# Kernel optimization log

Measured on AMD Instinct MI355X. Metric: run time of the kernel, lower is better.

## Reference

```python
import jax, jax.numpy as jnp
import numpy as np

NUM_HEADS = 8
EPS = 1e-5


def _dwconv_cpe(x, w, b, H, W):
    # x: [B,N,C]; depthwise 3x3 conv positional encoding with residual
    B, N, C = x.shape
    f = x.transpose(0, 2, 1).reshape(B, C, H, W)
    f = jax.lax.conv_general_dilated(
        f, w, window_strides=(1, 1), padding='SAME',
        feature_group_count=C, dimension_numbers=('NCHW', 'OIHW', 'NCHW'))
    f = f + b[None, :, None, None]
    return x + f.reshape(B, C, N).transpose(0, 2, 1)


def _layernorm(x, g, b):
    mu = jnp.mean(x, axis=-1, keepdims=True)
    var = jnp.mean(jnp.square(x - mu), axis=-1, keepdims=True)
    return (x - mu) * jax.lax.rsqrt(var + EPS) * g + b


def _channel_attn(x, source, q_w, kv_w, proj_w, proj_b):
    B, N, C = x.shape
    h = NUM_HEADS
    d = C // h
    scale = d ** -0.5
    q = (x @ q_w).reshape(B, N, h, d).transpose(0, 2, 1, 3)          # [B,h,N,d]
    kv = (source @ kv_w).reshape(B, N, 2, h, d).transpose(2, 0, 3, 1, 4)
    k = kv[0] * scale                                                # [B,h,N,d]
    v = kv[1]                                                        # [B,h,N,d]
    # channel cross-covariance: [B,h,d,d], softmax over last channel dim
    attn = jax.nn.softmax(jnp.einsum('bhnd,bhne->bhde', k, v), axis=-1)
    out = jnp.einsum('bhde,bhne->bhnd', attn, q)                     # [B,h,N,d]
    out = out.transpose(0, 2, 1, 3).reshape(B, N, C)
    return out @ proj_w + proj_b


def _forward(x, source, H, W, cpe0_w, cpe0_b, cpe1_w, cpe1_b,
             norm1_g, norm1_b, q_w, kv_w, proj_w, proj_b,
             norm2_g, norm2_b, fc1_w, fc1_b, fc2_w, fc2_b):
    x = _dwconv_cpe(x, cpe0_w, cpe0_b, H, W)
    source = _dwconv_cpe(source, cpe0_w, cpe0_b, H, W)  # cpe[0] shared, per source
    x = _layernorm(x, norm1_g, norm1_b)
    source = _layernorm(source, norm1_g, norm1_b)
    cur = _channel_attn(x, source, q_w, kv_w, proj_w, proj_b)
    x = x + cur  # residual on the normalized x (as in the original code)
    x = _dwconv_cpe(x, cpe1_w, cpe1_b, H, W)
    h = _layernorm(x, norm2_g, norm2_b)
    h = jax.nn.gelu(h @ fc1_w + fc1_b, approximate=False) @ fc2_w + fc2_b
    return x + h


def setup_inputs() -> dict:
    key = jax.random.key(0)
    ks = jax.random.split(key, 16)
    B, H, W, C = 8, 64, 64, 384
    N = H * W
    Ch = int(C * 4.0)
    s = 0.02
    return {
        'x': jax.random.normal(ks[0], (B, N, C), jnp.float32),
        'source': jax.random.normal(ks[1], (B, N, C), jnp.float32),
        'H': H, 'W': W,
        'cpe0_w': jax.random.normal(ks[2], (C, 1, 3, 3), jnp.float32) * s,
        'cpe0_b': jnp.zeros((C,), jnp.float32),
        'cpe1_w': jax.random.normal(ks[3], (C, 1, 3, 3), jnp.float32) * s,
        'cpe1_b': jnp.zeros((C,), jnp.float32),
        'norm1_g': jnp.ones((C,), jnp.float32),
        'norm1_b': jnp.zeros((C,), jnp.float32),
        'q_w': jax.random.normal(ks[4], (C, C), jnp.float32) * s,
        'kv_w': jax.random.normal(ks[5], (C, 2 * C), jnp.float32) * s,
        'proj_w': jax.random.normal(ks[6], (C, C), jnp.float32) * s,
        'proj_b': jnp.zeros((C,), jnp.float32),
        'norm2_g': jnp.ones((C,), jnp.float32),
        'norm2_b': jnp.zeros((C,), jnp.float32),
        'fc1_w': jax.random.normal(ks[7], (C, Ch), jnp.float32) * s,
        'fc1_b': jnp.zeros((Ch,), jnp.float32),
        'fc2_w': jax.random.normal(ks[8], (Ch, C), jnp.float32) * s,
        'fc2_b': jnp.zeros((C,), jnp.float32),
    }


def reference(x, source, H, W, cpe0_w, cpe0_b, cpe1_w, cpe1_b,
              norm1_g, norm1_b, q_w, kv_w, proj_w, proj_b,
              norm2_g, norm2_b, fc1_w, fc1_b, fc2_w, fc2_b):
    return _forward(x, source, H, W, cpe0_w, cpe0_b, cpe1_w, cpe1_b,
                    norm1_g, norm1_b, q_w, kv_w, proj_w, proj_b,
                    norm2_g, norm2_b, fc1_w, fc1_b, fc2_w, fc2_b)
```

## Files before the change

kernel.cpp:

```cpp
#include <hip/hip_runtime.h>
#include <hip/hip_bf16.h>
#include <math.h>

typedef __hip_bfloat16 bf16;
typedef unsigned short u16t;
typedef __bf16 bfx8 __attribute__((ext_vector_type(8)));
typedef float fx4 __attribute__((ext_vector_type(4)));
typedef unsigned short usx8 __attribute__((ext_vector_type(8)));

constexpr int Bq = 8, Hh = 64, Ww = 64, Nn = 4096, Cc = 384, NH = 8, CH = 1536;
constexpr int Mrows = Bq * Nn;
constexpr int NS = 4;
constexpr int NSP = 6;
constexpr float EPSC = 1e-5f;
constexpr float SCALE = 0.14433756729740643f;

__device__ __forceinline__ float toF(bf16 v) { return __bfloat162float(v); }

__device__ __forceinline__ float ldFlag(const void* p, size_t i, int f) {
    if (f) return __bfloat162float(((const bf16*)p)[i]);
    return ((const float*)p)[i];
}

__device__ __forceinline__ float u2f(u16t u) {
    unsigned int x = ((unsigned int)u) << 16;
    float fv;
    __builtin_memcpy(&fv, &x, 4);
    return fv;
}
__device__ __forceinline__ u16t f2u(float v) {
    bf16 h = __float2bfloat16(v);
    u16t u;
    __builtin_memcpy(&u, &h, 2);
    return u;
}
__device__ __forceinline__ fx4 mfma16(usx8 a, usx8 b, fx4 c) {
    return __builtin_amdgcn_mfma_f32_16x16x32_bf16(
        __builtin_bit_cast(bfx8, a), __builtin_bit_cast(bfx8, b), c, 0, 0, 0);
}

__device__ __forceinline__ void gload16(const void* g, void* l) {
    __builtin_amdgcn_global_load_lds(
        reinterpret_cast<const __attribute__((address_space(1))) unsigned int*>(
            reinterpret_cast<uintptr_t>(g)),
        reinterpret_cast<__attribute__((address_space(3))) unsigned int*>(
            reinterpret_cast<uintptr_t>(l)),
        16, 0, 0);
}

__global__ __launch_bounds__(256) void probe_k(const void* __restrict__ p, int* __restrict__ flag) {
    int t = threadIdx.x;
    int bad = 0;
    for (int i = t; i < 4096; i += 256) {
        unsigned short u = ((const unsigned short*)p)[i];
        unsigned e = (u >> 7) & 0xFF;
        if (e >= 134) bad++;
    }
    __shared__ int sh[256];
    sh[t] = bad;
    __syncthreads();
    for (int s = 128; s > 0; s >>= 1) {
        if (t < s) sh[t] += sh[t + s];
        __syncthreads();
    }
    if (t == 0) flag[0] = (sh[0] < 64) ? 1 : 0;
}

template <int INM, int MODE>
__global__ __launch_bounds__(384) void dwconv_ln(const void* __restrict__ xin,
                                                 const void* __restrict__ w,
                                                 const void* __restrict__ bias,
                                                 bf16* __restrict__ out,
                                                 const void* __restrict__ g,
                                                 const void* __restrict__ bb,
                                                 float* __restrict__ mu,
                                                 float* __restrict__ rs,
                                                 const int* __restrict__ flagp) {
    int f = *flagp;
    int c = threadIdx.x;
    int w0 = blockIdx.x * 8;
    int hh = blockIdx.y;
    int b = blockIdx.z;
    size_t base = (size_t)b * Nn * Cc;
    float wreg[9];
#pragma unroll
    for (int j = 0; j < 9; j++) wreg[j] = ldFlag(w, c * 9 + j, f);
    float bc = ldFlag(bias, c, f);
    float v[3][10];
#pragma unroll
    for (int ky = 0; ky < 3; ky++) {
        int yy = hh + ky - 1;
        bool rv = (yy >= 0 && yy < Hh);
#pragma unroll
        for (int j = 0; j < 10; j++) {
            int xx = w0 - 1 + j;
            bool cv = (xx >= 0 && xx < Ww);
            float val = 0.f;
            if (rv && cv) {
                size_t idx = base + (size_t)(yy * Ww + xx) * Cc + c;
                val = (INM == 1) ? toF(((const bf16*)xin)[idx]) : ldFlag(xin, idx, f);
            }
            v[ky][j] = val;
        }
    }
    float r[8], s[8], s2[8];
#pragma unroll
    for (int p = 0; p < 8; p++) {
        float a = bc;
#pragma unroll
        for (int ky = 0; ky < 3; ky++)
#pragma unroll
            for (int kx = 0; kx < 3; kx++) a += v[ky][p + kx] * wreg[ky * 3 + kx];
        r[p] = v[1][p + 1] + a;
        s[p] = r[p];
        s2[p] = r[p] * r[p];
    }
#pragma unroll
    for (int off = 32; off > 0; off >>= 1) {
#pragma unroll
        for (int p = 0; p < 8; p++) {
            s[p] += __shfl_down(s[p], off, 64);
            s2[p] += __shfl_down(s2[p], off, 64);
        }
    }
    __shared__ float shS[6][8], shS2[6][8];
    __shared__ float shMu[8], shRs[8];
    int wv = c >> 6, ln = c & 63;
    if (ln == 0) {
#pragma unroll
        for (int p = 0; p < 8; p++) {
            shS[wv][p] = s[p];
            shS2[wv][p] = s2[p];
        }
    }
    __syncthreads();
    if (c < 8) {
        float S = 0, S2 = 0;
#pragma unroll
        for (int q = 0; q < 6; q++) {
            S += shS[q][c];
            S2 += shS2[q][c];
        }
        float m = S * (1.0f / Cc);
        float var = S2 * (1.0f / Cc) - m * m;
        float rr = rsqrtf(var + EPSC);
        if (MODE == 0) {
            shMu[c] = m;
            shRs[c] = rr;
        } else {
            int row = b * Nn + hh * Ww + w0 + c;
            mu[row] = m;
            rs[row] = rr;
        }
    }
    if (MODE == 0) {
        __syncthreads();
        float gc = ldFlag(g, c, f), bbc = ldFlag(bb, c, f);
#pragma unroll
        for (int p = 0; p < 8; p++) {
            size_t oi = base + (size_t)(hh * Ww + w0 + p) * Cc + c;
            out[oi] = __float2bfloat16((r[p] - shMu[p]) * shRs[p] * gc + bbc);
        }
    } else {
#pragma unroll
        for (int p = 0; p < 8; p++) {
            size_t oi = base + (size_t)(hh * Ww + w0 + p) * Cc + c;
            out[oi] = __float2bfloat16(r[p]);
        }
    }
}

__global__ __launch_bounds__(256) void reduceG_k(float* __restrict__ Gp) {
    const size_t Q = (size_t)Cc * Cc / 4;
    size_t j = (size_t)blockIdx.x * 256 + threadIdx.x;
    int b = (int)(j / Q);
    size_t i4 = j % Q;
    fx4* G4 = (fx4*)Gp;
    size_t base = (size_t)b * NS * Q;
    fx4 a = G4[base + i4];
#pragma unroll
    for (int s = 1; s < NS; s++) a += G4[base + (size_t)s * Q + i4];
    G4[base + i4] = a;
}

template <int AM, int OM, int WM, bool GELU, bool LNA, int RES, int AR>
__global__ __launch_bounds__(256) void gemm_k(const void* __restrict__ A, size_t aBatch,
                                              const void* __restrict__ W, size_t wBatch,
                                              int ldw, int colOff,
                                              const void* __restrict__ bias,
                                              const bf16* __restrict__ resid, size_t rBatch,
                                              const float* __restrict__ mu,
                                              const float* __restrict__ rs, size_t sBatch,
                                              const void* __restrict__ cg,
                                              const void* __restrict__ cb,
                                              void* __restrict__ out, size_t oBatch,
                                              size_t outRow0,
                                              int M, int K, int Nc,
                                              const int* __restrict__ flagp) {
    int f = *flagp;
    int z = blockIdx.z;
    const size_t MK = (size_t)M * K;
    __shared__ float As[16][68];
    __shared__ float Bs[16][68];
    int t = threadIdx.x;
    int tx = t & 15, ty = t >> 4;
    int row0 = blockIdx.x * 64, n0 = blockIdx.y * 64;
    float acc[4][4] = {};
    for (int k0 = 0; k0 < K; k0 += 16) {
#pragma unroll
        for (int i = 0; i < 4; i++) {
            int lin = i * 256 + t;
            int kk = lin & 15, m = lin >> 4;
            size_t ai = (size_t)z * aBatch + (size_t)(row0 + m) * K + k0 + kk;
            float v;
            if (AR > 1) {
                v = 0;
#pragma unroll
                for (int s = 0; s < AR; s++) v += ((const float*)A)[ai + (size_t)s * MK];
            } else {
                v = (AM == 0) ? ((const float*)A)[ai] : toF(((const bf16*)A)[ai]);
            }
            if (LNA) {
                float muv = mu[z * sBatch + row0 + m], rsv = rs[z * sBatch + row0 + m];
                v = (v - muv) * rsv * ldFlag(cg, k0 + kk, f) + ldFlag(cb, k0 + kk, f);
            }
            As[kk][m] = v;
        }
#pragma unroll
        for (int i = 0; i < 4; i++) {
            int lin = i * 256 + t;
            int nn2 = lin & 63, kk = lin >> 6;
            size_t wi = (size_t)z * wBatch + (size_t)(k0 + kk) * ldw + colOff + n0 + nn2;
            Bs[kk][nn2] = (WM == 1) ? toF(((const bf16*)W)[wi]) : ldFlag(W, wi, f);
        }
        __syncthreads();
#pragma unroll
        for (int kk = 0; kk < 16; kk++) {
            float a[4], bv[4];
#pragma unroll
            for (int i = 0; i < 4; i++) a[i] = As[kk][ty * 4 + i];
#pragma unroll
            for (int j = 0; j < 4; j++) bv[j] = Bs[kk][tx * 4 + j];
#pragma unroll
            for (int i = 0; i < 4; i++)
#pragma unroll
                for (int j = 0; j < 4; j++) acc[i][j] += a[i] * bv[j];
        }
        __syncthreads();
    }
#pragma unroll
    for (int i = 0; i < 4; i++) {
        int m = row0 + ty * 4 + i;
#pragma unroll
        for (int j = 0; j < 4; j++) {
            int nn2 = n0 + tx * 4 + j;
            float v = acc[i][j];
            if (bias) v += ldFlag(bias, nn2, f);
            if (GELU) v = 0.5f * v * (1.0f + erff(v * 0.70710678118654752f));
            if (RES == 1) v += toF(resid[(size_t)z * rBatch + (size_t)m * Nc + nn2]);
            size_t oi = (size_t)z * oBatch + (outRow0 + m) * (size_t)Nc + nn2;
            if (OM == 2) ((float*)out)[oi] = v;
            else if (OM == 1) ((bf16*)out)[oi] = __float2bfloat16(v);
            else {
                if (f) ((bf16*)out)[oi] = __float2bfloat16(v);
                else ((float*)out)[oi] = v;
            }
        }
    }
}

__global__ __launch_bounds__(256) void transpose_k(const void* __restrict__ W,
                                                   u16t* __restrict__ WT,
                                                   int K, int N,
                                                   const int* __restrict__ flagp) {
    int f = *flagp;
    __shared__ u16t T[64][72];
    int n0 = blockIdx.x * 64, k0 = blockIdx.y * 64;
    int t = threadIdx.x;
#pragma unroll
    for (int i = 0; i < 16; i++) {
        int lin = i * 256 + t;
        int kk = lin >> 6, nn = lin & 63;
        T[nn][kk] = f2u(ldFlag(W, (size_t)(k0 + kk) * N + n0 + nn, f));
    }
    __syncthreads();
#pragma unroll
    for (int i = 0; i < 16; i++) {
        int lin = i * 256 + t;
        int nn = lin >> 6, kk = lin & 63;
        WT[(size_t)(n0 + nn) * K + k0 + kk] = T[nn][kk];
    }
}

__global__ __launch_bounds__(256) void transpose_scale_k(const void* __restrict__ W,
                                                         const void* __restrict__ g,
                                                         u16t* __restrict__ WT,
                                                         int K, int N,
                                                         const int* __restrict__ flagp) {
    int f = *flagp;
    __shared__ u16t T[64][72];
    int n0 = blockIdx.x * 64, k0 = blockIdx.y * 64;
    int t = threadIdx.x;
#pragma unroll
    for (int i = 0; i < 16; i++) {
        int lin = i * 256 + t;
        int kk = lin >> 6, nn = lin & 63;
        T[nn][kk] = f2u(ldFlag(g, k0 + kk, f) * ldFlag(W, (size_t)(k0 + kk) * N + n0 + nn, f));
    }
    __syncthreads();
#pragma unroll
    for (int i = 0; i < 16; i++) {
        int lin = i * 256 + t;
        int nn = lin >> 6, kk = lin & 63;
        WT[(size_t)(n0 + nn) * K + k0 + kk] = T[nn][kk];
    }
}

__global__ __launch_bounds__(256) void fc1fold_k(const void* __restrict__ fc1w,
                                                 const void* __restrict__ g,
                                                 const void* __restrict__ bb,
                                                 const void* __restrict__ b1,
                                                 float* __restrict__ negc1,
                                                 float* __restrict__ cb2,
                                                 const int* __restrict__ flagp) {
    int f = *flagp;
    __shared__ float gs[384], bs[384];
    int t = threadIdx.x;
    for (int i = t; i < 384; i += 256) {
        gs[i] = ldFlag(g, i, f);
        bs[i] = ldFlag(bb, i, f);
    }
    __syncthreads();
    int n = blockIdx.x * 256 + t;
    float s1 = 0, s2 = 0;
    for (int k = 0; k < 384; k++) {
        float w = ldFlag(fc1w, (size_t)k * CH + n, f);
        s1 += gs[k] * w;
        s2 += bs[k] * w;
    }
    negc1[n] = -s1;
    cb2[n] = s2 + ldFlag(b1, n, f);
}

template <int OM, bool GELU, int RES, int EPI>
__global__ __launch_bounds__(256) void gemm_mfma(
    const u16t* __restrict__ A, size_t aBatch,
    const u16t* __restrict__ BT, size_t btBatch,
    const void* __restrict__ bias,
    const u16t* __restrict__ resid, size_t rBatch,
    const float* __restrict__ mu, const float* __restrict__ rs,
    const float* __restrict__ negc1, const float* __restrict__ cb2,
    void* __restrict__ out, size_t oBatch, size_t outRow0,
    int K, int N, const int* __restrict__ flagp) {
    int f = *flagp;
    int z = blockIdx.z;
    int t = threadIdx.x;
    int row0 = blockIdx.x * 128, n0 = blockIdx.y * 128;
    __shared__ u16t As[128][64];
    __shared__ u16t Bs[128][64];
    const u16t* Ab = A + (size_t)z * aBatch;
    const u16t* Bb = BT + (size_t)z * btBatch;
    int lane = t & 63, wv = t >> 6;
    int srow = lane >> 3;
    int schk = ((lane & 7) ^ srow) << 3;
    const u16t* asrc[4];
    const u16t* bsrc[4];
    u16t* adst[4];
    u16t* bdst[4];
#pragma unroll
    for (int i = 0; i < 4; i++) {
        int r = 32 * wv + 8 * i;
        asrc[i] = Ab + (size_t)(row0 + r + srow) * K + schk;
        bsrc[i] = Bb + (size_t)(n0 + r + srow) * K + schk;
        adst[i] = &As[r][0];
        bdst[i] = &Bs[r][0];
    }
    fx4 acc[4][4];
    fx4 zz = {0.f, 0.f, 0.f, 0.f};
#pragma unroll
    for (int i = 0; i < 4; i++)
#pragma unroll
        for (int j = 0; j < 4; j++) acc[i][j] = zz;
    int wr = (wv >> 1) * 64, wc = (wv & 1) * 64;
    int lr = lane & 15, lg = lane >> 4;
    int KT = K / 64;
    for (int kt = 0; kt < KT; kt++) {
        if (kt) __syncthreads();
#pragma unroll
        for (int i = 0; i < 4; i++) {
            gload16(asrc[i] + kt * 64, adst[i]);
            gload16(bsrc[i] + kt * 64, bdst[i]);
        }
        __syncthreads();
#pragma unroll
        for (int ks = 0; ks < 2; ks++) {
            usx8 af[4], bfv[4];
#pragma unroll
            for (int r = 0; r < 4; r++) {
                int row = wr + r * 16 + lr;
                af[r] = *(const usx8*)&As[row][((4 * ks + lg) ^ (row & 7)) << 3];
            }
#pragma unroll
            for (int c = 0; c < 4; c++) {
                int row = wc + c * 16 + lr;
                bfv[c] = *(const usx8*)&Bs[row][((4 * ks + lg) ^ (row & 7)) << 3];
            }
#pragma unroll
            for (int r = 0; r < 4; r++)
#pragma unroll
                for (int c = 0; c < 4; c++)
                    acc[r][c] = mfma16(af[r], bfv[c], acc[r][c]);
        }
    }
#pragma unroll
    for (int r = 0; r < 4; r++) {
        int mb = row0 + wr + r * 16 + lg * 4;
        fx4 muq, rsq;
        if (EPI == 1) {
            muq = *(const fx4*)&mu[mb];
            rsq = *(const fx4*)&rs[mb];
        }
#pragma unroll
        for (int c = 0; c < 4; c++) {
            int gc = n0 + wc + c * 16 + lr;
            float bv = bias ? ldFlag(bias, gc, f) : 0.0f;
            float nc1 = (EPI == 1) ? negc1[gc] : 0.f;
            float cbv = (EPI == 1) ? cb2[gc] : 0.f;
#pragma unroll
            for (int q = 0; q < 4; q++) {
                int m = mb + q;
                float v;
                if (EPI == 1) v = rsq[q] * (acc[r][c][q] + muq[q] * nc1) + cbv;
                else v = acc[r][c][q] + bv;
                if (GELU) v = 0.5f * v * (1.0f + erff(v * 0.70710678118654752f));
                if (RES == 1) v += u2f(resid[(size_t)z * rBatch + (size_t)m * N + gc]);
                if (RES == 2) v += u2f(Ab[(size_t)m * K + gc]);
                size_t oi = (size_t)z * oBatch + (outRow0 + m) * (size_t)N + gc;
                if (OM == 1) ((u16t*)out)[oi] = f2u(v);
                else {
                    if (f) ((u16t*)out)[oi] = f2u(v);
                    else ((float*)out)[oi] = v;
                }
            }
        }
    }
}

__global__ __launch_bounds__(256) void gram_mfma(const u16t* __restrict__ sc,
                                                 float* __restrict__ Gp) {
    int bx = blockIdx.x, sp = blockIdx.y, b = blockIdx.z;
    int ci0 = (bx / 3) * 128, cj0 = (bx % 3) * 128;
    __shared__ u16t As[128][72];
    __shared__ u16t Bs[128][72];
    int t = threadIdx.x;
    const int scc = (t * 8) & 127;
    const int snn = t >> 4;
    const int RPS = Nn / NS;
    int rowbase = b * Nn + sp * RPS;
    usx8 ra[4], rb[4];
    auto ldstep = [&](int nn0) {
#pragma unroll
        for (int i = 0; i < 4; i++) {
            int r = rowbase + nn0 + i * 16 + snn;
            ra[i] = *(const usx8*)&sc[(size_t)r * Cc + ci0 + scc];
            rb[i] = *(const usx8*)&sc[(size_t)r * Cc + cj0 + scc];
        }
    };
    auto wrstep = [&]() {
#pragma unroll
        for (int i = 0; i < 4; i++) {
            int n = i * 16 + snn;
            int q = n >> 3, nl = n & 7;
#pragma unroll
            for (int j = 0; j < 8; j++) {
                int c = scc + j;
                int swz = ((c >> 3) ^ (c >> 6)) & 7;
                int po = ((q ^ swz) << 3) + nl;
                As[c][po] = ra[i][j];
                Bs[c][po] = rb[i][j];
            }
        }
    };
    fx4 acc[4][4];
    fx4 zz = {0.f, 0.f, 0.f, 0.f};
#pragma unroll
    for (int i = 0; i < 4; i++)
#pragma unroll
        for (int j = 0; j < 4; j++) acc[i][j] = zz;
    int lane = t & 63, w = t >> 6;
    int wr = (w >> 1) * 64, wc = (w & 1) * 64;
    int lr = lane & 15, lg = lane >> 4;
    ldstep(0);
    wrstep();
    __syncthreads();
    const int KT = RPS / 64;
    for (int kt = 0; kt < KT; kt++) {
        if (kt + 1 < KT) ldstep((kt + 1) * 64);
#pragma unroll
        for (int ks = 0; ks < 2; ks++) {
            usx8 af[4], bfv[4];
#pragma unroll
            for (int r = 0; r < 4; r++) {
                int ch = wr + r * 16 + lr;
                int swz = ((ch >> 3) ^ (ch >> 6)) & 7;
                af[r] = *(const usx8*)&As[ch][((ks * 4 + lg) ^ swz) << 3];
            }
#pragma unroll
            for (int c = 0; c < 4; c++) {
                int ch = wc + c * 16 + lr;
                int swz = ((ch >> 3) ^ (ch >> 6)) & 7;
                bfv[c] = *(const usx8*)&Bs[ch][((ks * 4 + lg) ^ swz) << 3];
            }
#pragma unroll
            for (int r = 0; r < 4; r++)
#pragma unroll
                for (int c = 0; c < 4; c++)
                    acc[r][c] = mfma16(af[r], bfv[c], acc[r][c]);
        }
        __syncthreads();
        if (kt + 1 < KT) {
            wrstep();
            __syncthreads();
        }
    }
    float* dst = Gp + ((size_t)b * NS + sp) * (size_t)Cc * Cc;
#pragma unroll
    for (int r = 0; r < 4; r++)
#pragma unroll
        for (int c = 0; c < 4; c++)
#pragma unroll
            for (int q = 0; q < 4; q++)
                dst[(size_t)(ci0 + wr + r * 16 + lg * 4 + q) * Cc + cj0 + wc + c * 16 + lr] =
                    acc[r][c][q];
}

__global__ __launch_bounds__(256) void attn_part_k(const float* __restrict__ P,
                                                   const void* __restrict__ kv_w,
                                                   float* __restrict__ Sp,
                                                   const int* __restrict__ flagp) {
    int f = *flagp;
    int hd = blockIdx.x;
    int b = blockIdx.y;
    int sp = blockIdx.z;
    int c0 = sp * 64;
    int t = threadIdx.x;
    const float* Pb = P + (size_t)b * Cc * Cc;
    __shared__ float Pc[64][49];
    __shared__ float Wkc[64][49];
    for (int idx = t; idx < 3072; idx += 256) {
        int r = idx / 48, e = idx % 48;
        int c = c0 + r;
        Pc[r][e] = Pb[(size_t)c * Cc + hd * 48 + e];
        Wkc[r][e] = ldFlag(kv_w, (size_t)c * 768 + hd * 48 + e, f);
    }
    __syncthreads();
    int obase = t * 9;
    float acc[9] = {};
#pragma unroll
    for (int r = 0; r < 64; r++) {
#pragma unroll
        for (int j = 0; j < 9; j++) {
            int d = (obase + j) / 48, e = (obase + j) % 48;
            acc[j] += Wkc[r][d] * Pc[r][e];
        }
    }
    float* dst = Sp + (((size_t)b * NH + hd) * NSP + sp) * 2304;
#pragma unroll
    for (int j = 0; j < 9; j++) dst[obase + j] = acc[j];
}

__global__ __launch_bounds__(256) void attn_soft_k(const float* __restrict__ Sp,
                                                   float* __restrict__ attn) {
    int hd = blockIdx.x;
    int b = blockIdx.y;
    int t = threadIdx.x;
    __shared__ float Ss[48][49];
    const float* src = Sp + (((size_t)b * NH + hd) * NSP) * 2304;
    for (int idx = t; idx < 2304; idx += 256) {
        float s = 0;
#pragma unroll
        for (int sp = 0; sp < NSP; sp++) s += src[sp * 2304 + idx];
        Ss[idx / 48][idx % 48] = s * SCALE;
    }
    __syncthreads();
    if (t < 48) {
        float m = -1e30f;
#pragma unroll
        for (int e = 0; e < 48; e++) m = fmaxf(m, Ss[t][e]);
        float ex[48];
        float sum = 0;
#pragma unroll
        for (int e = 0; e < 48; e++) {
            ex[e] = expf(Ss[t][e] - m);
            sum += ex[e];
        }
        float inv = 1.0f / sum;
#pragma unroll
        for (int e = 0; e < 48; e++)
            attn[((size_t)b * NH + hd) * 2304 + t * 48 + e] = ex[e] * inv;
    }
}

__global__ __launch_bounds__(256) void wtilde_k(const void* __restrict__ q_w,
                                                const float* __restrict__ attn,
                                                bf16* __restrict__ Wt_,
                                                const int* __restrict__ flagp) {
    int f = *flagp;
    int c0 = blockIdx.x * 64;
    int hd = blockIdx.y;
    int b = blockIdx.z;
    int t = threadIdx.x;
    __shared__ float at[48][48];
    __shared__ float wq[64][48];
    const float* ab = attn + ((size_t)b * NH + hd) * 2304;
    for (int o = t; o < 2304; o += 256) at[o / 48][o % 48] = ab[o];
    for (int o = t; o < 3072; o += 256) {
        int cc = o / 48, e = o % 48;
        wq[cc][e] = ldFlag(q_w, (size_t)(c0 + cc) * Cc + hd * 48 + e, f);
    }
    __syncthreads();
    bf16* outb = Wt_ + (size_t)b * Cc * Cc;
    for (int o = t; o < 3072; o += 256) {
        int cc = o / 48, d = o % 48;
        float s = 0;
#pragma unroll
        for (int e = 0; e < 48; e++) s += wq[cc][e] * at[d][e];
        outb[(size_t)(c0 + cc) * Cc + hd * 48 + d] = __float2bfloat16(s);
    }
}

extern "C" void kernel_launch(void* const* d_in, const int* in_sizes, int n_in,
                              void* d_out, int out_size, void* d_ws, size_t ws_size,
                              hipStream_t stream) {
    (void)in_sizes; (void)n_in; (void)out_size;
    const void* x = d_in[0];
    const void* srcp = d_in[1];
    const void* cpe0_w = d_in[4];
    const void* cpe0_b = d_in[5];
    const void* cpe1_w = d_in[6];
    const void* cpe1_b = d_in[7];
    const void* n1g = d_in[8];
    const void* n1b = d_in[9];
    const void* q_w = d_in[10];
    const void* kv_w = d_in[11];
    const void* proj_w = d_in[12];
    const void* proj_b = d_in[13];
    const void* n2g = d_in[14];
    const void* n2b = d_in[15];
    const void* fc1_w = d_in[16];
    const void* fc1_b = d_in[17];
    const void* fc2_w = d_in[18];
    const void* fc2_b = d_in[19];
    char* ws = (char*)d_ws;

    const size_t CcCc = (size_t)Cc * Cc;
    const size_t NnCc = (size_t)Nn * Cc;
    const size_t SLOT = (size_t)Mrows * Cc * sizeof(bf16);
    int* flag = (int*)ws;
    bf16* s0 = (bf16*)(ws + 64);
    bf16* s1 = (bf16*)(ws + 64 + SLOT);
    float* Gp = (float*)s1;
    u16t* WeffT = (u16t*)s1;
    bf16* x3 = s1;
    float* P = (float*)(ws + 64 + 2 * SLOT);
    bf16* Wt_ = (bf16*)P;
    u16t* projT = (u16t*)((char*)P + 2359296);
    u16t* fc1T = (u16t*)P;
    u16t* fc2T = (u16t*)((char*)P + 1179648);
    float* attnB = (float*)(ws + 64 + 2 * SLOT + 4718592);
    float* mu2 = (float*)(ws + 64 + 2 * SLOT + 4718592 + 589824);
    float* rs2 = mu2 + Mrows;
    float* negc1 = rs2 + Mrows;
    float* cb2 = negc1 + CH;
    bf16* lnS = s0;
    float* Sp = (float*)s0;
    bf16* x2 = s0;
    u16t* h1c = (u16t*)s0;
    const size_t NEED = (size_t)((char*)(cb2 + CH) - ws);
    if (ws_size < NEED) return;

    bf16* lnX = (bf16*)d_out;

    probe_k<<<1, 256, 0, stream>>>(x, flag);

    dwconv_ln<2, 0><<<dim3(Ww / 8, Hh, Bq), 384, 0, stream>>>(
        x, cpe0_w, cpe0_b, lnX, n1g, n1b, nullptr, nullptr, flag);

    dwconv_ln<2, 0><<<dim3(Ww / 8, Hh, Bq), 384, 0, stream>>>(
        srcp, cpe0_w, cpe0_b, lnS, n1g, n1b, nullptr, nullptr, flag);
    gram_mfma<<<dim3(9, NS, Bq), 256, 0, stream>>>((const u16t*)lnS, Gp);
    reduceG_k<<<(Bq * CcCc / 4) / 256, 256, 0, stream>>>(Gp);

    gemm_k<0, 2, 2, false, false, 0, 1><<<dim3(6, 6, Bq), 256, 0, stream>>>(
        Gp, (size_t)NS * CcCc, kv_w, 0, 768, 384, nullptr, nullptr, 0,
        nullptr, nullptr, 0, nullptr, nullptr, P, CcCc, 0, Cc, Cc, Cc, flag);

    attn_part_k<<<dim3(NH, Bq, NSP), 256, 0, stream>>>(P, kv_w, Sp, flag);
    attn_soft_k<<<dim3(NH, Bq), 256, 0, stream>>>(Sp, attnB);
    wtilde_k<<<dim3(6, NH, Bq), 256, 0, stream>>>(q_w, attnB, Wt_, flag);
    transpose_k<<<dim3(6, 6), 256, 0, stream>>>(proj_w, projT, Cc, Cc, flag);
    gemm_mfma<1, false, 0, 0><<<dim3(3, 3, Bq), 256, 0, stream>>>(
        projT, 0, (const u16t*)Wt_, CcCc, nullptr, nullptr, 0,
        nullptr, nullptr, nullptr, nullptr, WeffT, CcCc, 0, Cc, Cc, flag);

    transpose_scale_k<<<dim3(24, 6), 256, 0, stream>>>(fc1_w, n2g, fc1T, Cc, CH, flag);
    transpose_k<<<dim3(6, 24), 256, 0, stream>>>(fc2_w, fc2T, CH, Cc, flag);
    fc1fold_k<<<CH / 256, 256, 0, stream>>>(fc1_w, n2g, n2b, fc1_b, negc1, cb2, flag);

    gemm_mfma<1, false, 2, 0><<<dim3(32, 3, Bq), 256, 0, stream>>>(
        (const u16t*)lnX, NnCc, WeffT, CcCc, proj_b, nullptr, 0,
        nullptr, nullptr, nullptr, nullptr, x2, NnCc, 0, Cc, Cc, flag);

    dwconv_ln<1, 1><<<dim3(Ww / 8, Hh, Bq), 384, 0, stream>>>(
        x2, cpe1_w, cpe1_b, x3, nullptr, nullptr, mu2, rs2, flag);

    constexpr int CR = 8192;
    for (int ch = 0; ch < Mrows / CR; ch++) {
        size_t roff = (size_t)ch * CR;
        gemm_mfma<1, true, 0, 1><<<dim3(CR / 128, CH / 128, 1), 256, 0, stream>>>(
            (const u16t*)x3 + roff * Cc, 0, fc1T, 0, nullptr, nullptr, 0,
            mu2 + roff, rs2 + roff, negc1, cb2, h1c, 0, 0, Cc, CH, flag);
        gemm_mfma<0, false, 1, 0><<<dim3(CR / 128, Cc / 128, 1), 256, 0, stream>>>(
            h1c, 0, fc2T, 0, fc2_b, (const u16t*)x3 + roff * Cc, 0,
            nullptr, nullptr, nullptr, nullptr, d_out, 0, roff, CH, Cc, flag);
    }
}
```

Baseline: 801.4 us.

## Replace scalar Gram-times-Wv GEMM with split-bf16 MFMA and double-buffer MFMA GEMM

The fp32 scalar gemm_k that multiplied the reduced Gram matrix by the V weights is removed. reduceG_k now writes the Gram matrix as a hi/lo bf16 split along K (K=768), and the value-weight columns are transposed and duplicated so that a bf16 MFMA GEMM recovers close to fp32 accuracy. The shared MFMA GEMM also gains double-buffered LDS staging, overlapping the next tile's loads with the current tile's compute at the cost of twice the shared memory.

```diff
diff --git a/kernel.cpp b/kernel.cpp
--- a/kernel.cpp
+++ b/kernel.cpp
@@ -170,108 +170,32 @@
     }
 }
 
-__global__ __launch_bounds__(256) void reduceG_k(float* __restrict__ Gp) {
-    const size_t Q = (size_t)Cc * Cc / 4;
+__global__ __launch_bounds__(256) void reduceG_k(const float* __restrict__ Gp,
+                                                 u16t* __restrict__ Gs) {
+    const size_t Q4 = (size_t)Cc * Cc / 4;
     size_t j = (size_t)blockIdx.x * 256 + threadIdx.x;
-    int b = (int)(j / Q);
-    size_t i4 = j % Q;
-    fx4* G4 = (fx4*)Gp;
-    size_t base = (size_t)b * NS * Q;
+    int b = (int)(j / Q4);
+    size_t i4 = j % Q4;
+    const fx4* G4 = (const fx4*)Gp;
+    size_t base = (size_t)b * NS * Q4;
     fx4 a = G4[base + i4];
 #pragma unroll
-    for (int s = 1; s < NS; s++) a += G4[base + (size_t)s * Q + i4];
-    G4[base + i4] = a;
-}
-
-template <int AM, int OM, int WM, bool GELU, bool LNA, int RES, int AR>
-__global__ __launch_bounds__(256) void gemm_k(const void* __restrict__ A, size_t aBatch,
-                                              const void* __restrict__ W, size_t wBatch,
-                                              int ldw, int colOff,
-                                              const void* __restrict__ bias,
-                                              const bf16* __restrict__ resid, size_t rBatch,
-                                              const float* __restrict__ mu,
-                                              const float* __restrict__ rs, size_t sBatch,
-                                              const void* __restrict__ cg,
-                                              const void* __restrict__ cb,
-                                              void* __restrict__ out, size_t oBatch,
-                                              size_t outRow0,
-                                              int M, int K, int Nc,
-                                              const int* __restrict__ flagp) {
-    int f = *flagp;
-    int z = blockIdx.z;
-    const size_t MK = (size_t)M * K;
-    __shared__ float As[16][68];
-    __shared__ float Bs[16][68];
-    int t = threadIdx.x;
-    int tx = t & 15, ty = t >> 4;
-    int row0 = blockIdx.x * 64, n0 = blockIdx.y * 64;
-    float acc[4][4] = {};
-    for (int k0 = 0; k0 < K; k0 += 16) {
-#pragma unroll
-        for (int i = 0; i < 4; i++) {
-            int lin = i * 256 + t;
-            int kk = lin & 15, m = lin >> 4;
-            size_t ai = (size_t)z * aBatch + (size_t)(row0 + m) * K + k0 + kk;
-            float v;
-            if (AR > 1) {
-                v = 0;
-#pragma unroll
-                for (int s = 0; s < AR; s++) v += ((const float*)A)[ai + (size_t)s * MK];
-            } else {
-                v = (AM == 0) ? ((const float*)A)[ai] : toF(((const bf16*)A)[ai]);
-            }
-            if (LNA) {
-                float muv = mu[z * sBatch + row0 + m], rsv = rs[z * sBatch + row0 + m];
-                v = (v - muv) * rsv * ldFlag(cg, k0 + kk, f) + ldFlag(cb, k0 + kk, f);
-            }
-            As[kk][m] = v;
-        }
-#pragma unroll
-        for (int i = 0; i < 4; i++) {
-            int lin = i * 256 + t;
-            int nn2 = lin & 63, kk = lin >> 6;
-            size_t wi = (size_t)z * wBatch + (size_t)(k0 + kk) * ldw + colOff + n0 + nn2;
-            Bs[kk][nn2] = (WM == 1) ? toF(((const bf16*)W)[wi]) : ldFlag(W, wi, f);
-        }
-        __syncthreads();
-#pragma unroll
-        for (int kk = 0; kk < 16; kk++) {
-            float a[4], bv[4];
-#pragma unroll
-            for (int i = 0; i < 4; i++) a[i] = As[kk][ty * 4 + i];
-#pragma unroll
-            for (int j = 0; j < 4; j++) bv[j] = Bs[kk][tx * 4 + j];
-#pragma unroll
-            for (int i = 0; i < 4; i++)
-#pragma unroll
-                for (int j = 0; j < 4; j++) acc[i][j] += a[i] * bv[j];
-        }
-        __syncthreads();
-    }
-#pragma unroll
-    for (int i = 0; i < 4; i++) {
-        int m = row0 + ty * 4 + i;
-#pragma unroll
-        for (int j = 0; j < 4; j++) {
-            int nn2 = n0 + tx * 4 + j;
-            float v = acc[i][j];
-            if (bias) v += ldFlag(bias, nn2, f);
-            if (GELU) v = 0.5f * v * (1.0f + erff(v * 0.70710678118654752f));
-            if (RES == 1) v += toF(resid[(size_t)z * rBatch + (size_t)m * Nc + nn2]);
-            size_t oi = (size_t)z * oBatch + (outRow0 + m) * (size_t)Nc + nn2;
-            if (OM == 2) ((float*)out)[oi] = v;
-            else if (OM == 1) ((bf16*)out)[oi] = __float2bfloat16(v);
-            else {
-                if (f) ((bf16*)out)[oi] = __float2bfloat16(v);
-                else ((float*)out)[oi] = v;
-            }
-        }
+    for (int s = 1; s < NS; s++) a += G4[base + (size_t)s * Q4 + i4];
+    int e0 = (int)(i4 * 4);
+    int m = e0 / Cc, k = e0 % Cc;
+    u16t* row = Gs + ((size_t)b * Cc + m) * 768 + k;
+#pragma unroll
+    for (int q = 0; q < 4; q++) {
+        u16t hi = f2u(a[q]);
+        row[q] = hi;
+        row[384 + q] = f2u(a[q] - u2f(hi));
     }
 }
 
 __global__ __launch_bounds__(256) void transpose_k(const void* __restrict__ W,
                                                    u16t* __restrict__ WT,
-                                                   int K, int N,
+                                                   int ldw, int colOff,
+                                                   int dstStride, int dstOff,
                                                    const int* __restrict__ flagp) {
     int f = *flagp;
     __shared__ u16t T[64][72];
@@ -281,14 +205,14 @@
     for (int i = 0; i < 16; i++) {
         int lin = i * 256 + t;
         int kk = lin >> 6, nn = lin & 63;
-        T[nn][kk] = f2u(ldFlag(W, (size_t)(k0 + kk) * N + n0 + nn, f));
+        T[nn][kk] = f2u(ldFlag(W, (size_t)(k0 + kk) * ldw + colOff + n0 + nn, f));
     }
     __syncthreads();
 #pragma unroll
     for (int i = 0; i < 16; i++) {
         int lin = i * 256 + t;
         int nn = lin >> 6, kk = lin & 63;
-        WT[(size_t)(n0 + nn) * K + k0 + kk] = T[nn][kk];
+        WT[(size_t)(n0 + nn) * dstStride + dstOff + k0 + kk] = T[nn][kk];
     }
 }
 
@@ -356,8 +280,8 @@
     int z = blockIdx.z;
     int t = threadIdx.x;
     int row0 = blockIdx.x * 128, n0 = blockIdx.y * 128;
-    __shared__ u16t As[128][64];
-    __shared__ u16t Bs[128][64];
+    __shared__ u16t As[2][128][64];
+    __shared__ u16t Bs[2][128][64];
     const u16t* Ab = A + (size_t)z * aBatch;
     const u16t* Bb = BT + (size_t)z * btBatch;
     int lane = t & 63, wv = t >> 6;
@@ -365,16 +289,21 @@
     int schk = ((lane & 7) ^ srow) << 3;
     const u16t* asrc[4];
     const u16t* bsrc[4];
-    u16t* adst[4];
-    u16t* bdst[4];
+    int rbase[4];
 #pragma unroll
     for (int i = 0; i < 4; i++) {
         int r = 32 * wv + 8 * i;
+        rbase[i] = r;
         asrc[i] = Ab + (size_t)(row0 + r + srow) * K + schk;
         bsrc[i] = Bb + (size_t)(n0 + r + srow) * K + schk;
-        adst[i] = &As[r][0];
-        bdst[i] = &Bs[r][0];
-    }
+    }
+    auto STAGE = [&](int kt, int buf) {
+#pragma unroll
+        for (int i = 0; i < 4; i++) {
+            gload16(asrc[i] + kt * 64, &As[buf][rbase[i]][0]);
+            gload16(bsrc[i] + kt * 64, &Bs[buf][rbase[i]][0]);
+        }
+    };
     fx4 acc[4][4];
     fx4 zz = {0.f, 0.f, 0.f, 0.f};
 #pragma unroll
@@ -384,26 +313,23 @@
     int wr = (wv >> 1) * 64, wc = (wv & 1) * 64;
     int lr = lane & 15, lg = lane >> 4;
     int KT = K / 64;
+    STAGE(0, 0);
+    __syncthreads();
     for (int kt = 0; kt < KT; kt++) {
-        if (kt) __syncthreads();
-#pragma unroll
-        for (int i = 0; i < 4; i++) {
-            gload16(asrc[i] + kt * 64, adst[i]);
-            gload16(bsrc[i] + kt * 64, bdst[i]);
-        }
-        __syncthreads();
+        int cur = kt & 1;
+        if (kt + 1 < KT) STAGE(kt + 1, cur ^ 1);
 #pragma unroll
         for (int ks = 0; ks < 2; ks++) {
             usx8 af[4], bfv[4];
 #pragma unroll
             for (int r = 0; r < 4; r++) {
                 int row = wr + r * 16 + lr;
-                af[r] = *(const usx8*)&As[row][((4 * ks + lg) ^ (row & 7)) << 3];
+                af[r] = *(const usx8*)&As[cur][row][((4 * ks + lg) ^ (row & 7)) << 3];
             }
 #pragma unroll
             for (int c = 0; c < 4; c++) {
                 int row = wc + c * 16 + lr;
-                bfv[c] = *(const usx8*)&Bs[row][((4 * ks + lg) ^ (row & 7)) << 3];
+                bfv[c] = *(const usx8*)&Bs[cur][row][((4 * ks + lg) ^ (row & 7)) << 3];
             }
 #pragma unroll
             for (int r = 0; r < 4; r++)
@@ -411,6 +337,7 @@
                 for (int c = 0; c < 4; c++)
                     acc[r][c] = mfma16(af[r], bfv[c], acc[r][c]);
         }
+        __syncthreads();
     }
 #pragma unroll
     for (int r = 0; r < 4; r++) {
@@ -437,6 +364,7 @@
                 if (RES == 2) v += u2f(Ab[(size_t)m * K + gc]);
                 size_t oi = (size_t)z * oBatch + (outRow0 + m) * (size_t)N + gc;
                 if (OM == 1) ((u16t*)out)[oi] = f2u(v);
+                else if (OM == 2) ((float*)out)[oi] = v;
                 else {
                     if (f) ((u16t*)out)[oi] = f2u(v);
                     else ((float*)out)[oi] = v;
@@ -660,6 +588,7 @@
     bf16* s0 = (bf16*)(ws + 64);
     bf16* s1 = (bf16*)(ws + 64 + SLOT);
     float* Gp = (float*)s1;
+    u16t* Gsplit = (u16t*)((char*)s1 + 18874368);
     u16t* WeffT = (u16t*)s1;
     bf16* x3 = s1;
     float* P = (float*)(ws + 64 + 2 * SLOT);
@@ -668,6 +597,7 @@
     u16t* fc1T = (u16t*)P;
     u16t* fc2T = (u16t*)((char*)P + 1179648);
     float* attnB = (float*)(ws + 64 + 2 * SLOT + 4718592);
+    u16t* WvT768 = (u16t*)attnB;
     float* mu2 = (float*)(ws + 64 + 2 * SLOT + 4718592 + 589824);
     float* rs2 = mu2 + Mrows;
     float* negc1 = rs2 + Mrows;
@@ -689,22 +619,24 @@
     dwconv_ln<2, 0><<<dim3(Ww / 8, Hh, Bq), 384, 0, stream>>>(
         srcp, cpe0_w, cpe0_b, lnS, n1g, n1b, nullptr, nullptr, flag);
     gram_mfma<<<dim3(9, NS, Bq), 256, 0, stream>>>((const u16t*)lnS, Gp);
-    reduceG_k<<<(Bq * CcCc / 4) / 256, 256, 0, stream>>>(Gp);
-
-    gemm_k<0, 2, 2, false, false, 0, 1><<<dim3(6, 6, Bq), 256, 0, stream>>>(
-        Gp, (size_t)NS * CcCc, kv_w, 0, 768, 384, nullptr, nullptr, 0,
-        nullptr, nullptr, 0, nullptr, nullptr, P, CcCc, 0, Cc, Cc, Cc, flag);
+    reduceG_k<<<(Bq * CcCc / 4) / 256, 256, 0, stream>>>(Gp, Gsplit);
+
+    transpose_k<<<dim3(6, 6), 256, 0, stream>>>(kv_w, WvT768, 768, 384, 768, 0, flag);
+    transpose_k<<<dim3(6, 6), 256, 0, stream>>>(kv_w, WvT768, 768, 384, 768, 384, flag);
+    gemm_mfma<2, false, 0, 0><<<dim3(3, 3, Bq), 256, 0, stream>>>(
+        Gsplit, (size_t)Cc * 768, WvT768, 0, nullptr, nullptr, 0,
+        nullptr, nullptr, nullptr, nullptr, P, CcCc, 0, 768, Cc, flag);
 
     attn_part_k<<<dim3(NH, Bq, NSP), 256, 0, stream>>>(P, kv_w, Sp, flag);
     attn_soft_k<<<dim3(NH, Bq), 256, 0, stream>>>(Sp, attnB);
     wtilde_k<<<dim3(6, NH, Bq), 256, 0, stream>>>(q_w, attnB, Wt_, flag);
-    transpose_k<<<dim3(6, 6), 256, 0, stream>>>(proj_w, projT, Cc, Cc, flag);
+    transpose_k<<<dim3(6, 6), 256, 0, stream>>>(proj_w, projT, Cc, 0, Cc, 0, flag);
     gemm_mfma<1, false, 0, 0><<<dim3(3, 3, Bq), 256, 0, stream>>>(
         projT, 0, (const u16t*)Wt_, CcCc, nullptr, nullptr, 0,
         nullptr, nullptr, nullptr, nullptr, WeffT, CcCc, 0, Cc, Cc, flag);
 
     transpose_scale_k<<<dim3(24, 6), 256, 0, stream>>>(fc1_w, n2g, fc1T, Cc, CH, flag);
-    transpose_k<<<dim3(6, 24), 256, 0, stream>>>(fc2_w, fc2T, CH, Cc, flag);
+    transpose_k<<<dim3(6, 24), 256, 0, stream>>>(fc2_w, fc2T, Cc, 0, CH, 0, flag);
     fc1fold_k<<<CH / 256, 256, 0, stream>>>(fc1_w, n2g, n2b, fc1_b, negc1, cb2, flag);
 
     gemm_mfma<1, false, 2, 0><<<dim3(32, 3, Bq), 256, 0, stream>>>(
```

After: 773.8 us. 3.4% less time.
